# Kernel tuning notes

Measured on AMD Instinct MI355X. Metric: run time of the kernel, lower is better.

Reference implementation:

```python
import jax, jax.numpy as jnp
import numpy as np

N_NODES = 100000
N_EDGES = 1600000
HIDDEN = 64
N_LAYERS = 3
N_CLASSES = 2
N_GRAPHS = 128
NEG_SLOPE = 0.2  # PyG GATConv default negative_slope


def setup_inputs() -> dict:
    key = jax.random.key(0)
    ks = jax.random.split(key, 8)
    x = jax.random.randint(ks[0], (N_NODES,), 0, 2)
    edge_index = jax.random.randint(ks[1], (2, N_EDGES), 0, N_NODES)
    batch = jnp.sort(jax.random.randint(ks[2], (N_NODES,), 0, N_GRAPHS))
    scale = 1.0 / np.sqrt(HIDDEN)
    embed_table = jax.random.normal(ks[3], (2, HIDDEN), jnp.float32)
    Ws = jax.random.normal(ks[4], (N_LAYERS, HIDDEN, HIDDEN), jnp.float32) * scale
    a_srcs = jax.random.normal(ks[5], (N_LAYERS, HIDDEN), jnp.float32) * scale
    a_dsts = jax.random.normal(ks[6], (N_LAYERS, HIDDEN), jnp.float32) * scale
    biases = jnp.zeros((N_LAYERS, HIDDEN), jnp.float32)
    W_out = jax.random.normal(ks[7], (HIDDEN, N_CLASSES), jnp.float32) * scale
    b_out = jnp.zeros((N_CLASSES,), jnp.float32)
    return {"x": x, "edge_index": edge_index, "batch": batch,
            "embed_table": embed_table, "Ws": Ws, "a_srcs": a_srcs,
            "a_dsts": a_dsts, "biases": biases, "W_out": W_out, "b_out": b_out}


def _gat_layer(h, src, dst, W, a_s, a_d, b):
    # h: [N, D]; src/dst: [E'] (self loops included) -> PyG GATConv, heads=1
    hW = h @ W                                   # [N, D]
    e = jax.nn.leaky_relu((hW @ a_s)[src] + (hW @ a_d)[dst], NEG_SLOPE)  # [E']
    m = jax.ops.segment_max(e, dst, num_segments=N_NODES)               # stable softmax per dst
    ex = jnp.exp(e - m[dst])
    denom = jax.ops.segment_sum(ex, dst, num_segments=N_NODES)
    alpha = ex / denom[dst]                      # [E']
    out = jax.ops.segment_sum(hW[src] * alpha[:, None], dst, num_segments=N_NODES)
    return out + b


def reference(x, edge_index, batch, embed_table, Ws, a_srcs, a_dsts, biases, W_out, b_out):
    loop = jnp.arange(N_NODES)
    src = jnp.concatenate([edge_index[0], loop])  # PyG add_self_loops=True
    dst = jnp.concatenate([edge_index[1], loop])
    h = embed_table[x]                            # [N, D]
    for l in range(N_LAYERS):
        h = _gat_layer(h, src, dst, Ws[l], a_srcs[l], a_dsts[l], biases[l])
        if l < N_LAYERS - 1:
            h = jax.nn.relu(h)
    sums = jax.ops.segment_sum(h, batch, num_segments=N_GRAPHS)
    counts = jax.ops.segment_sum(jnp.ones((N_NODES,), h.dtype), batch, num_segments=N_GRAPHS)
    pooled = sums / jnp.maximum(counts, 1.0)[:, None]  # global_mean_pool
    return pooled @ W_out + b_out                      # [G, num_classes]
```

## Files before the change

kernel.cpp:

```cpp
#include <hip/hip_runtime.h>
#include <hip/hip_bf16.h>
#include <float.h>

#define N_NODES 100000
#define N_EDGES 1600000
#define HIDDEN 64
#define N_GRAPHS 128
#define NEG_SLOPE 0.2f
#define ETOT (N_EDGES + N_NODES)

#define BSHIFT 9
#define NB ((N_NODES + 511) >> BSHIFT)
#define PAIR_CHUNK 4096
#define PAIR_BLOCKS ((N_EDGES + PAIR_CHUNK - 1) / PAIR_CHUNK)
#define XBIT_BLOCKS ((N_NODES + 255) / 256)
#define TBL_BLOCKS (NLVL / 4)
#define CAP 12288

#define NREP 64
#define REP_STRIDE 272
#define NLVL 512

__device__ __forceinline__ unsigned short f2bf(float f) {
    unsigned u = __float_as_uint(f);
    unsigned r = (u + 0x7FFFu + ((u >> 16) & 1u)) >> 16;
    return (unsigned short)r;
}
__device__ __forceinline__ float blo(unsigned u) { return __uint_as_float(u << 16); }
__device__ __forceinline__ float bhi(unsigned u) { return __uint_as_float(u & 0xFFFF0000u); }
__device__ __forceinline__ int sb0(unsigned u) { return (int)((unsigned)(u << 24)) >> 24; }
__device__ __forceinline__ int sb1(unsigned u) { return (int)((unsigned)(u << 16)) >> 24; }
__device__ __forceinline__ int sb2(unsigned u) { return (int)((unsigned)(u << 8)) >> 24; }
__device__ __forceinline__ int sb3(unsigned u) { return (int)u >> 24; }


__global__ __launch_bounds__(256) void k_prep(
    const int* __restrict__ x,
    const float* __restrict__ embed, const float* __restrict__ Ws,
    const float* __restrict__ biases, const float* __restrict__ a_srcs,
    const float* __restrict__ a_dsts, const float* __restrict__ W_out,
    int* __restrict__ gcnt, float* __restrict__ pool_acc,
    unsigned* __restrict__ xb,
    unsigned char* __restrict__ Tq8, float* __restrict__ Tscl,
    float* __restrict__ Ts1s, float* __restrict__ Ts1d,
    float* __restrict__ sparams)
{
    int t = threadIdx.x, b = blockIdx.x;

    if (b < TBL_BLOCKS) {
        if (b == 0 && t < NB) gcnt[t] = 0;
        if (b < NREP && t < 2 * N_GRAPHS) pool_acc[b * REP_STRIDE + t] = 0.f;

        int l = b * 4 + (t >> 6);
        int f = t & 63;
        float r0 = 0.f, r1 = 0.f;
#pragma unroll 8
        for (int k = 0; k < 64; ++k) {
            float w = Ws[k * 64 + f];
            r0 = fmaf(embed[k], w, r0);
            r1 = fmaf(embed[64 + k], w, r1);
        }
        if (l == 0) {
            float as = a_srcs[f], ad = a_dsts[f];
            float t0 = r0 * as, t1 = r1 * as, t2 = r0 * ad, t3 = r1 * ad;
#pragma unroll
            for (int off = 32; off >= 1; off >>= 1) {
                t0 += __shfl_xor(t0, off); t1 += __shfl_xor(t1, off);
                t2 += __shfl_xor(t2, off); t3 += __shfl_xor(t3, off);
            }
            if (f == 0) { sparams[0] = t0; sparams[1] = t1; sparams[2] = t2; sparams[3] = t3; }
        }
        if (l == 1) {
            float b2 = biases[128 + f];
            float t4 = b2 * W_out[f * 2];
            float t5 = b2 * W_out[f * 2 + 1];
#pragma unroll
            for (int off = 32; off >= 1; off >>= 1) {
                t4 += __shfl_xor(t4, off); t5 += __shfl_xor(t5, off);
            }
            if (f == 0) { sparams[4] = t4; sparams[5] = t5; }
        }
        float c1 = (float)l * (1.f / (NLVL - 1));
        float o = fmaxf(biases[f] + r0 + c1 * (r1 - r0), 0.f);
        const float* W1 = Ws + 4096;
        float h = 0.f;
#pragma unroll 8
        for (int k = 0; k < 64; ++k) h = fmaf(__shfl(o, k), W1[k * 64 + f], h);
        float ss = h * a_srcs[64 + f];
        float sd = h * a_dsts[64 + f];
        float am = fabsf(h);
#pragma unroll
        for (int off = 32; off >= 1; off >>= 1) {
            ss += __shfl_xor(ss, off);
            sd += __shfl_xor(sd, off);
            am = fmaxf(am, __shfl_xor(am, off));
        }
        float iscl = (am > 0.f) ? 127.f / am : 0.f;
        Tq8[l * 64 + f] = (unsigned char)(__float2int_rn(h * iscl) & 255);
        if (f == 0) { Tscl[l] = am * (1.f / 127.f); Ts1s[l] = ss; Ts1d[l] = sd; }
    } else {
        int i = (b - TBL_BLOCKS) * 256 + t;
        int lane = t & 63;
        bool bb = (i < N_NODES) && (x[i] != 0);
        unsigned long long m = __ballot(bb);
        int wid = i >> 6;
        if (i < N_NODES + 64) {
            if (lane == 0) xb[wid * 2] = (unsigned)m;
            if (lane == 32) xb[wid * 2 + 1] = (unsigned)(m >> 32);
        }
    }
}


__global__ __launch_bounds__(256) void k_scatter(
    const int* __restrict__ e0, const int* __restrict__ e1,
    const unsigned* __restrict__ xb, int* __restrict__ gcnt,
    int* __restrict__ pairs)
{
    __shared__ int hcnt[NB];
    __shared__ int base[NB];
    __shared__ int lstart[NB];
    __shared__ int tot[256];
    __shared__ int staged[PAIR_CHUNK];
    __shared__ int sdest[PAIR_CHUNK];
    int t = threadIdx.x, b = blockIdx.x;
    if (t < NB) hcnt[t] = 0;
    __syncthreads();
    int ebase = b * PAIR_CHUNK;
    int ecount = min(PAIR_CHUNK, N_EDGES - ebase);
    for (int i = 4 * t; i < ecount; i += 1024) {
        int4 d4 = *(const int4*)(e1 + ebase + i);
        atomicAdd(&hcnt[d4.x >> BSHIFT], 1);
        atomicAdd(&hcnt[d4.y >> BSHIFT], 1);
        atomicAdd(&hcnt[d4.z >> BSHIFT], 1);
        atomicAdd(&hcnt[d4.w >> BSHIFT], 1);
    }
    __syncthreads();
    int v = (t < NB) ? hcnt[t] : 0;
    tot[t] = v;
    __syncthreads();
    for (int off = 1; off < 256; off <<= 1) {
        int u = (t >= off) ? tot[t - off] : 0;
        __syncthreads();
        tot[t] += u;
        __syncthreads();
    }
    if (t < NB) {
        lstart[t] = tot[t] - v;
        base[t] = v ? atomicAdd(&gcnt[t], v) : 0;
        hcnt[t] = 0;
    }
    __syncthreads();
    for (int i = 4 * t; i < ecount; i += 1024) {
        int4 s4 = *(const int4*)(e0 + ebase + i);
        int4 d4 = *(const int4*)(e1 + ebase + i);
        int ss[4] = {s4.x, s4.y, s4.z, s4.w};
        int dd[4] = {d4.x, d4.y, d4.z, d4.w};
#pragma unroll
        for (int j = 0; j < 4; ++j) {
            int s = ss[j], d = dd[j];
            int xv = (xb[s >> 5] >> (s & 31)) & 1;
            int B = d >> BSHIFT;
            int idx = atomicAdd(&hcnt[B], 1);
            int lp = lstart[B] + idx;
            staged[lp] = (xv << 26) | ((d & 511) << 17) | s;
            sdest[lp] = B * CAP + base[B] + idx;
        }
    }
    __syncthreads();
    for (int i = t; i < ecount; i += 256)
        pairs[sdest[i]] = staged[i];
}

__global__ __launch_bounds__(1024) void k_csr_bucket(
    const int* __restrict__ pairs, const int* __restrict__ gcnt,
    const int* __restrict__ x, const float* __restrict__ sparams,
    int* __restrict__ rowptr, int* __restrict__ col,
    unsigned short* __restrict__ cidx)
{
    __shared__ int deg[512];
    __shared__ int excl[512];
    __shared__ int cnt2[512];
    __shared__ int wsum[16];
    __shared__ int p0sh;
    int b = blockIdx.x;
    int t = threadIdx.x;
    int nb = b << BSHIFT;
    int nodes = min(512, N_NODES - nb);

    int pv = (t < b) ? gcnt[t] : 0;
#pragma unroll
    for (int off = 32; off >= 1; off >>= 1) pv += __shfl_xor(pv, off);
    if ((t & 63) == 0) wsum[t >> 6] = pv;
    __syncthreads();
    if (t == 0) {
        int s = 0;
#pragma unroll
        for (int i = 0; i < 16; ++i) s += wsum[i];
        p0sh = s;
    }

    int xself = 0;
    if (t < 512) {
        xself = (t < nodes) ? (x[nb + t] & 1) : 0;
        deg[t] = (t < nodes) ? (1 | (xself << 16)) : 0;
        cnt2[t] = 1;
    }
    __syncthreads();
    int cnt = gcnt[b];
    int pbase = b * CAP;
    for (int i = t; i < cnt; i += 1024) {
        int p = pairs[pbase + i];
        atomicAdd(&deg[(p >> 17) & 511], 1 | (((p >> 26) & 1) << 16));
    }
    __syncthreads();

    int packed = (t < 512) ? deg[t] : 0;
    int val = packed & 0xFFFF;
    int kx = packed >> 16;
    if (t < nodes) {
        float ss0 = sparams[0], ss1 = sparams[1];
        float sd = xself ? sparams[3] : sparams[2];
        float e0 = ss0 + sd; e0 = (e0 >= 0.f) ? e0 : NEG_SLOPE * e0;
        float e1 = ss1 + sd; e1 = (e1 >= 0.f) ? e1 : NEG_SLOPE * e1;
        float pp0 = __expf(e0), pp1 = __expf(e1);
        float kn = (float)kx, dn = (float)(val - kx);
        float c1 = kn * pp1 / (dn * pp0 + kn * pp1);
        cidx[nb + t] = (unsigned short)__float2int_rn(c1 * (float)(NLVL - 1));
    }

    int xx = val;
#pragma unroll
    for (int off = 1; off < 64; off <<= 1) {
        int y = __shfl_up(xx, off);
        if ((t & 63) >= off) xx += y;
    }
    if ((t & 63) == 63 && t < 512) wsum[t >> 6] = xx;
    __syncthreads();
    if (t == 0) {
        int s = 0;
#pragma unroll
        for (int i = 0; i < 8; ++i) { int v = wsum[i]; wsum[i] = s; s += v; }
    }
    __syncthreads();
    int ex = xx - val + wsum[t >> 6];
    if (t < 512) excl[t] = ex;

    int p0 = p0sh;
    int colbase = p0 + nb;
    if (t < nodes) {
        rowptr[nb + t] = colbase + ex;
        col[colbase + ex] = nb + t;
    }
    if (b == NB - 1 && t == 0) rowptr[N_NODES] = ETOT;
    __syncthreads();
    for (int i = t; i < cnt; i += 1024) {
        int p = pairs[pbase + i];
        int li = (p >> 17) & 511;
        int pos = colbase + excl[li] + atomicAdd(&cnt2[li], 1);
        col[pos] = p & 0x1FFFF;
    }
}


__global__ __launch_bounds__(256) void k_agg1(
    const unsigned char* __restrict__ Tq8, const float* __restrict__ Tscl,
    const float* __restrict__ Ts1s, const float* __restrict__ Ts1d,
    const unsigned short* __restrict__ cidx, const int* __restrict__ col,
    const int* __restrict__ rowptr, const float* __restrict__ bias,
    unsigned short* __restrict__ hout)
{
    __shared__ float2 stash[4][64];
    int t = threadIdx.x;
    int wave = t >> 6, lane = t & 63;
    int h = lane >> 5, hl = lane & 31;
    int base = blockIdx.x * 8 + wave * 2;
    if (base >= N_NODES) return;
    const char* hb = (const char*)Tq8;

    int node = base + h;
    bool valid = (node < N_NODES);
    int row = 0, end = 0;
    if (valid) { row = rowptr[node]; end = rowptr[node + 1]; }
    int deg = end - row;
    int degO = __shfl_xor(deg, 32);
    bool fast = (deg <= 32) && (degO <= 32);

    if (fast) {
        int idx = 0;
        float p = 0.f, sc = 0.f;
        if (hl < deg) idx = cidx[col[row + hl]];
        float sdi = Ts1d[__shfl(idx, h * 32)];
        if (hl < deg) {
            float ee = Ts1s[idx] + sdi;
            ee = (ee >= 0.f) ? ee : NEG_SLOPE * ee;
            p = __expf(ee);
            sc = Tscl[idx];
        }
        stash[wave][lane] = make_float2(p * sc, __int_as_float(idx * 64));

        int q = hl >> 4;
        int f = hl & 15;
        int f4 = f * 4;
        int sb = h * 32;
        float a0 = 0.f, a1 = 0.f, a2 = 0.f, a3 = 0.f;
        int degr = (deg + 7) & ~7;
        for (int j = q; j < degr; j += 8) {
            float2 e0 = stash[wave][sb + j];
            float2 e1 = stash[wave][sb + j + 2];
            float2 e2 = stash[wave][sb + j + 4];
            float2 e3 = stash[wave][sb + j + 6];
            unsigned v0 = *(const unsigned*)(hb + (__float_as_int(e0.y) + f4));
            unsigned v1 = *(const unsigned*)(hb + (__float_as_int(e1.y) + f4));
            unsigned v2 = *(const unsigned*)(hb + (__float_as_int(e2.y) + f4));
            unsigned v3 = *(const unsigned*)(hb + (__float_as_int(e3.y) + f4));
            a0 = fmaf(e0.x, (float)sb0(v0), a0);
            a1 = fmaf(e0.x, (float)sb1(v0), a1);
            a2 = fmaf(e0.x, (float)sb2(v0), a2);
            a3 = fmaf(e0.x, (float)sb3(v0), a3);
            a0 = fmaf(e1.x, (float)sb0(v1), a0);
            a1 = fmaf(e1.x, (float)sb1(v1), a1);
            a2 = fmaf(e1.x, (float)sb2(v1), a2);
            a3 = fmaf(e1.x, (float)sb3(v1), a3);
            a0 = fmaf(e2.x, (float)sb0(v2), a0);
            a1 = fmaf(e2.x, (float)sb1(v2), a1);
            a2 = fmaf(e2.x, (float)sb2(v2), a2);
            a3 = fmaf(e2.x, (float)sb3(v2), a3);
            a0 = fmaf(e3.x, (float)sb0(v3), a0);
            a1 = fmaf(e3.x, (float)sb1(v3), a1);
            a2 = fmaf(e3.x, (float)sb2(v3), a2);
            a3 = fmaf(e3.x, (float)sb3(v3), a3);
        }
        float denom = p;
#pragma unroll
        for (int off = 16; off >= 1; off >>= 1) denom += __shfl_xor(denom, off);
        float inv = 1.f / denom;
        a0 += __shfl_xor(a0, 16);
        a1 += __shfl_xor(a1, 16);
        a2 += __shfl_xor(a2, 16);
        a3 += __shfl_xor(a3, 16);
        if (hl < 16 && valid) {
            float4 bb = *(const float4*)&bias[4 * f];
            ushort4 pk;
            pk.x = f2bf(fmaxf(fmaf(a0, inv, bb.x), 0.f));
            pk.y = f2bf(fmaxf(fmaf(a1, inv, bb.y), 0.f));
            pk.z = f2bf(fmaxf(fmaf(a2, inv, bb.z), 0.f));
            pk.w = f2bf(fmaxf(fmaf(a3, inv, bb.w), 0.f));
            *(ushort4*)&hout[node * 64 + 4 * f] = pk;
        }
    } else {
        for (int s = 0; s < 2; ++s) {
            int nd = base + s;
            if (nd >= N_NODES) continue;
            int r = rowptr[nd], e = rowptr[nd + 1];
            float sdi = Ts1d[cidx[nd]];
            float m = -FLT_MAX;
            for (int j = r + lane; j < e; j += 64) {
                float ee = Ts1s[cidx[col[j]]] + sdi;
                ee = (ee >= 0.f) ? ee : NEG_SLOPE * ee;
                m = fmaxf(m, ee);
            }
#pragma unroll
            for (int off = 32; off >= 1; off >>= 1) m = fmaxf(m, __shfl_xor(m, off));
            float denom = 0.f;
            for (int j = r + lane; j < e; j += 64) {
                float ee = Ts1s[cidx[col[j]]] + sdi;
                ee = (ee >= 0.f) ? ee : NEG_SLOPE * ee;
                denom += __expf(ee - m);
            }
#pragma unroll
            for (int off = 32; off >= 1; off >>= 1) denom += __shfl_xor(denom, off);
            float inv = 1.f / denom;
            float acc = 0.f;
            for (int j = r; j < e; ++j) {
                int idxj = cidx[col[j]];
                float ee = Ts1s[idxj] + sdi;
                ee = (ee >= 0.f) ? ee : NEG_SLOPE * ee;
                float w = __expf(ee - m) * inv * Tscl[idxj];
                int bq = (int)(signed char)Tq8[idxj * 64 + lane];
                acc = fmaf(w, (float)bq, acc);
            }
            hout[nd * 64 + lane] = f2bf(fmaxf(acc + bias[lane], 0.f));
        }
    }
}


__global__ __launch_bounds__(256) void k_gemm2(
    const unsigned* __restrict__ h32, const float* __restrict__ W,
    const float* __restrict__ a_s, const float* __restrict__ a_d,
    const float* __restrict__ W_out,
    float4* __restrict__ szz)
{
    __shared__ float Wl[64 * 64];
    __shared__ float hT[64 * 68];
    int t = threadIdx.x;
    int r0 = blockIdx.x * 64;

    for (int i = t; i < 4096; i += 256) Wl[i] = W[i];
    for (int i = t; i < 2048; i += 256) {
        int r = i >> 5, m = i & 31;
        int row = r0 + r;
        unsigned u = (row < N_NODES) ? h32[row * 32 + m] : 0u;
        hT[(2 * m) * 68 + r]     = blo(u);
        hT[(2 * m + 1) * 68 + r] = bhi(u);
    }
    __syncthreads();

    int tcol = t & 15;
    int trow = t >> 4;
    float acc[4][4];
#pragma unroll
    for (int i = 0; i < 4; ++i)
#pragma unroll
        for (int j = 0; j < 4; ++j) acc[i][j] = 0.f;

    for (int k = 0; k < 64; ++k) {
        float4 va = *(const float4*)&hT[k * 68 + trow * 4];
        float4 vb = *(const float4*)&Wl[k * 64 + tcol * 4];
        float a[4] = {va.x, va.y, va.z, va.w};
        float bb[4] = {vb.x, vb.y, vb.z, vb.w};
#pragma unroll
        for (int i = 0; i < 4; ++i)
#pragma unroll
            for (int j = 0; j < 4; ++j) acc[i][j] = fmaf(a[i], bb[j], acc[i][j]);
    }

    float4 as4 = *(const float4*)&a_s[tcol * 4];
    float4 ad4 = *(const float4*)&a_d[tcol * 4];
    float asr[4] = {as4.x, as4.y, as4.z, as4.w};
    float adr[4] = {ad4.x, ad4.y, ad4.z, ad4.w};
    float4 wa = *(const float4*)&W_out[8 * tcol];
    float4 wb = *(const float4*)&W_out[8 * tcol + 4];

#pragma unroll
    for (int i = 0; i < 4; ++i) {
        int row = r0 + trow * 4 + i;
        float ps = 0.f, pd = 0.f;
#pragma unroll
        for (int j = 0; j < 4; ++j) {
            ps = fmaf(acc[i][j], asr[j], ps);
            pd = fmaf(acc[i][j], adr[j], pd);
        }
        float z0 = acc[i][0] * wa.x + acc[i][1] * wa.z + acc[i][2] * wb.x + acc[i][3] * wb.z;
        float z1 = acc[i][0] * wa.y + acc[i][1] * wa.w + acc[i][2] * wb.y + acc[i][3] * wb.w;
#pragma unroll
        for (int off = 8; off >= 1; off >>= 1) {
            ps += __shfl_xor(ps, off);
            pd += __shfl_xor(pd, off);
            z0 += __shfl_xor(z0, off);
            z1 += __shfl_xor(z1, off);
        }
        if (row < N_NODES && tcol == 0) {
            szz[row] = make_float4(ps, z0, z1, pd);
        }
    }
}


__global__ __launch_bounds__(256) void k_pool2(
    const float4* __restrict__ szz, const int* __restrict__ col,
    const int* __restrict__ rowptr, const int* __restrict__ batch,
    float* __restrict__ pool_acc)
{
    __shared__ int rp2[33];
    int t = threadIdx.x;
    int wave = t >> 6, lane = t & 63;
    int h = lane >> 5, hl = lane & 31;
    int nb0 = blockIdx.x * 32;
    if (t < 33) {
        int n = nb0 + t;
        rp2[t] = (n <= N_NODES) ? rowptr[n] : ETOT;
    }
    __syncthreads();
    float* rep = pool_acc + ((blockIdx.x * 4 + wave) & (NREP - 1)) * REP_STRIDE;

    int gcur = -1;
    float acc0 = 0.f, acc1 = 0.f;

#pragma unroll
    for (int i = 0; i < 4; ++i) {
        int nls = wave * 8 + 2 * i + h;
        int node = nb0 + nls;
        bool valid = (node < N_NODES);
        int row = valid ? rp2[nls] : 0;
        int end = valid ? rp2[nls + 1] : 0;
        int deg = end - row;
        int degO = __shfl_xor(deg, 32);
        bool fast = (deg <= 32) && (degO <= 32);
        float r0 = 0.f, r1 = 0.f;

        if (fast) {
            float sdi = valid ? szz[node].w : 0.f;
            float p = 0.f, zy = 0.f, zz = 0.f;
            if (hl < deg) {
                int c = col[row + hl];
                float4 sz = szz[c];
                float ee = sz.x + sdi;
                ee = (ee >= 0.f) ? ee : NEG_SLOPE * ee;
                p = __expf(ee);
                zy = sz.y; zz = sz.z;
            }
            float n0 = p * zy, n1 = p * zz, dn = p;
#pragma unroll
            for (int off = 16; off >= 1; off >>= 1) {
                n0 += __shfl_xor(n0, off);
                n1 += __shfl_xor(n1, off);
                dn += __shfl_xor(dn, off);
            }
            float inv = 1.f / dn;
            r0 = n0 * inv; r1 = n1 * inv;
        } else {
            float rr0[2], rr1[2];
#pragma unroll
            for (int s = 0; s < 2; ++s) {
                rr0[s] = rr1[s] = 0.f;
                int nds = wave * 8 + 2 * i + s;
                int nd = nb0 + nds;
                if (nd >= N_NODES) continue;
                int r = rp2[nds], e = rp2[nds + 1];
                float sdi = szz[nd].w;
                float n0 = 0.f, n1 = 0.f, dn = 0.f;
                for (int j = r + lane; j < e; j += 64) {
                    int c = col[j];
                    float4 sz = szz[c];
                    float ee = sz.x + sdi;
                    ee = (ee >= 0.f) ? ee : NEG_SLOPE * ee;
                    float p = __expf(ee);
                    n0 = fmaf(p, sz.y, n0);
                    n1 = fmaf(p, sz.z, n1);
                    dn += p;
                }
#pragma unroll
                for (int off = 32; off >= 1; off >>= 1) {
                    n0 += __shfl_xor(n0, off);
                    n1 += __shfl_xor(n1, off);
                    dn += __shfl_xor(dn, off);
                }
                float inv = 1.f / dn;
                rr0[s] = n0 * inv; rr1[s] = n1 * inv;
            }
            r0 = rr0[h]; r1 = rr1[h];
        }

        if (hl == 0 && valid) {
            int g = batch[node];
            if (g != gcur) {
                if (gcur >= 0) {
                    atomicAdd(&rep[gcur * 2], acc0);
                    atomicAdd(&rep[gcur * 2 + 1], acc1);
                }
                gcur = g; acc0 = r0; acc1 = r1;
            } else {
                acc0 += r0; acc1 += r1;
            }
        }
    }
    if (hl == 0 && gcur >= 0) {
        atomicAdd(&rep[gcur * 2], acc0);
        atomicAdd(&rep[gcur * 2 + 1], acc1);
    }
}


__device__ __forceinline__ int lower_bound_dev(const int* __restrict__ a, int n, int v) {
    int lo = 0, hi = n;
    while (lo < hi) {
        int mid = (lo + hi) >> 1;
        if (a[mid] < v) lo = mid + 1; else hi = mid;
    }
    return lo;
}

__global__ void k_head(const float* __restrict__ pool_acc,
                       const int* __restrict__ batch,
                       const float* __restrict__ b_out,
                       const float* __restrict__ sparams,
                       float* __restrict__ out)
{
    int t = threadIdx.x;
    if (t < 2 * N_GRAPHS) {
        float s = 0.f;
#pragma unroll 8
        for (int r = 0; r < NREP; ++r) s += pool_acc[r * REP_STRIDE + t];
        int g = t >> 1, c = t & 1;
        int start = lower_bound_dev(batch, N_NODES, g);
        int end = lower_bound_dev(batch, N_NODES, g + 1);
        float cnt = fmaxf((float)(end - start), 1.f);
        out[t] = s / cnt + sparams[4 + c] + b_out[c];
    }
}


extern "C" void kernel_launch(void* const* d_in, const int* in_sizes, int n_in,
                              void* d_out, int out_size, void* d_ws, size_t ws_size,
                              hipStream_t stream) {
    const int*   x       = (const int*)d_in[0];
    const int*   edge    = (const int*)d_in[1];
    const int*   batch   = (const int*)d_in[2];
    const float* embed   = (const float*)d_in[3];
    const float* Ws      = (const float*)d_in[4];
    const float* a_srcs  = (const float*)d_in[5];
    const float* a_dsts  = (const float*)d_in[6];
    const float* biases  = (const float*)d_in[7];
    const float* W_out   = (const float*)d_in[8];
    const float* b_out   = (const float*)d_in[9];
    float* out = (float*)d_out;

    char* ws = (char*)d_ws;
    size_t off = 0;
    auto alloc = [&](size_t bytes) -> void* {
        void* p = ws + off;
        off += (bytes + 255) & ~(size_t)255;
        return p;
    };
    unsigned short* hout  = (unsigned short*)alloc((size_t)N_NODES * 64 * sizeof(unsigned short));
    float4* szz     = (float4*)alloc((size_t)N_NODES * sizeof(float4));
    unsigned short* cidx = (unsigned short*)alloc((size_t)N_NODES * sizeof(unsigned short));
    int*   rowptr   = (int*)alloc((size_t)(N_NODES + 1) * sizeof(int));
    int*   colA     = (int*)alloc((size_t)ETOT * sizeof(int));
    int*   gcnt     = (int*)alloc((size_t)NB * sizeof(int));
    float* pool_acc = (float*)alloc((size_t)(NREP * REP_STRIDE) * sizeof(float));
    unsigned* xb    = (unsigned*)alloc((size_t)3232 * sizeof(unsigned));
    unsigned char* Tq8 = (unsigned char*)alloc((size_t)NLVL * 64);
    float* Tscl     = (float*)alloc((size_t)NLVL * sizeof(float));
    float* Ts1s     = (float*)alloc((size_t)NLVL * sizeof(float));
    float* Ts1d     = (float*)alloc((size_t)NLVL * sizeof(float));
    float* sparams  = (float*)alloc((size_t)8 * sizeof(float));
    int*   pairs    = (int*)alloc((size_t)NB * CAP * sizeof(int));

    const int* e0 = edge;
    const int* e1 = edge + N_EDGES;

    k_prep<<<TBL_BLOCKS + XBIT_BLOCKS, 256, 0, stream>>>(
        x, embed, Ws, biases, a_srcs, a_dsts, W_out,
        gcnt, pool_acc, xb, Tq8, Tscl, Ts1s, Ts1d, sparams);
    k_scatter<<<PAIR_BLOCKS, 256, 0, stream>>>(e0, e1, xb, gcnt, pairs);
    k_csr_bucket<<<NB, 1024, 0, stream>>>(pairs, gcnt, x, sparams, rowptr, colA, cidx);

    k_agg1<<<(N_NODES + 7) / 8, 256, 0, stream>>>(
        Tq8, Tscl, Ts1s, Ts1d, cidx, colA, rowptr, biases + 64, hout);
    k_gemm2<<<(N_NODES + 63) / 64, 256, 0, stream>>>(
        (const unsigned*)hout, Ws + 8192, a_srcs + 128, a_dsts + 128, W_out, szz);
    k_pool2<<<(N_NODES + 31) / 32, 256, 0, stream>>>(
        szz, colA, rowptr, batch, pool_acc);
    k_head<<<1, 256, 0, stream>>>(pool_acc, batch, b_out, sparams, out);
}
```

Before: 203.3 us.

## Move table precompute into scatter kernel, widen scatter blocks, vectorize bucket reads

The layer-1 lookup table computation moves out of k_prep into extra blocks of k_scatter, leaving k_prep to do only zeroing and bit-packing. k_scatter now runs 512-thread blocks over each 4096-edge chunk. k_csr_bucket reads the pairs array as int4 in both passes. The aim is to take the table work off the critical path ahead of scatter, and to cut per-thread loop iterations and load instructions, at the cost of higher per-block shared-memory atomic contention.

```diff
diff --git a/kernel.cpp b/kernel.cpp
--- a/kernel.cpp
+++ b/kernel.cpp
@@ -14,7 +14,7 @@
 #define PAIR_CHUNK 4096
 #define PAIR_BLOCKS ((N_EDGES + PAIR_CHUNK - 1) / PAIR_CHUNK)
 #define XBIT_BLOCKS ((N_NODES + 255) / 256)
-#define TBL_BLOCKS (NLVL / 4)
+#define TBL_BLOCKS (NLVL / 8)
 #define CAP 12288
 
 #define NREP 64
@@ -36,22 +36,45 @@
 
 __global__ __launch_bounds__(256) void k_prep(
     const int* __restrict__ x,
+    int* __restrict__ gcnt, float* __restrict__ pool_acc,
+    unsigned* __restrict__ xb)
+{
+    int t = threadIdx.x, b = blockIdx.x;
+    if (b == 0 && t < NB) gcnt[t] = 0;
+    if (b < NREP && t < 2 * N_GRAPHS) pool_acc[b * REP_STRIDE + t] = 0.f;
+    int i = b * 256 + t;
+    int lane = t & 63;
+    bool bb = (i < N_NODES) && (x[i] != 0);
+    unsigned long long m = __ballot(bb);
+    int wid = i >> 6;
+    if (i < N_NODES + 64) {
+        if (lane == 0) xb[wid * 2] = (unsigned)m;
+        if (lane == 32) xb[wid * 2 + 1] = (unsigned)(m >> 32);
+    }
+}
+
+
+__global__ __launch_bounds__(512) void k_scatter(
+    const int* __restrict__ e0, const int* __restrict__ e1,
+    const unsigned* __restrict__ xb, int* __restrict__ gcnt,
+    int* __restrict__ pairs,
     const float* __restrict__ embed, const float* __restrict__ Ws,
     const float* __restrict__ biases, const float* __restrict__ a_srcs,
     const float* __restrict__ a_dsts, const float* __restrict__ W_out,
-    int* __restrict__ gcnt, float* __restrict__ pool_acc,
-    unsigned* __restrict__ xb,
     unsigned char* __restrict__ Tq8, float* __restrict__ Tscl,
     float* __restrict__ Ts1s, float* __restrict__ Ts1d,
     float* __restrict__ sparams)
 {
+    __shared__ int hcnt[NB];
+    __shared__ int base[NB];
+    __shared__ int lstart[NB];
+    __shared__ int tot[256];
+    __shared__ int staged[PAIR_CHUNK];
+    __shared__ int sdest[PAIR_CHUNK];
     int t = threadIdx.x, b = blockIdx.x;
 
-    if (b < TBL_BLOCKS) {
-        if (b == 0 && t < NB) gcnt[t] = 0;
-        if (b < NREP && t < 2 * N_GRAPHS) pool_acc[b * REP_STRIDE + t] = 0.f;
-
-        int l = b * 4 + (t >> 6);
+    if (b >= PAIR_BLOCKS) {
+        int l = (b - PAIR_BLOCKS) * 8 + (t >> 6);
         int f = t & 63;
         float r0 = 0.f, r1 = 0.f;
 #pragma unroll 8
@@ -98,37 +121,14 @@
         float iscl = (am > 0.f) ? 127.f / am : 0.f;
         Tq8[l * 64 + f] = (unsigned char)(__float2int_rn(h * iscl) & 255);
         if (f == 0) { Tscl[l] = am * (1.f / 127.f); Ts1s[l] = ss; Ts1d[l] = sd; }
-    } else {
-        int i = (b - TBL_BLOCKS) * 256 + t;
-        int lane = t & 63;
-        bool bb = (i < N_NODES) && (x[i] != 0);
-        unsigned long long m = __ballot(bb);
-        int wid = i >> 6;
-        if (i < N_NODES + 64) {
-            if (lane == 0) xb[wid * 2] = (unsigned)m;
-            if (lane == 32) xb[wid * 2 + 1] = (unsigned)(m >> 32);
-        }
-    }
-}
-
-
-__global__ __launch_bounds__(256) void k_scatter(
-    const int* __restrict__ e0, const int* __restrict__ e1,
-    const unsigned* __restrict__ xb, int* __restrict__ gcnt,
-    int* __restrict__ pairs)
-{
-    __shared__ int hcnt[NB];
-    __shared__ int base[NB];
-    __shared__ int lstart[NB];
-    __shared__ int tot[256];
-    __shared__ int staged[PAIR_CHUNK];
-    __shared__ int sdest[PAIR_CHUNK];
-    int t = threadIdx.x, b = blockIdx.x;
+        return;
+    }
+
     if (t < NB) hcnt[t] = 0;
     __syncthreads();
     int ebase = b * PAIR_CHUNK;
     int ecount = min(PAIR_CHUNK, N_EDGES - ebase);
-    for (int i = 4 * t; i < ecount; i += 1024) {
+    for (int i = 4 * t; i < ecount; i += 2048) {
         int4 d4 = *(const int4*)(e1 + ebase + i);
         atomicAdd(&hcnt[d4.x >> BSHIFT], 1);
         atomicAdd(&hcnt[d4.y >> BSHIFT], 1);
@@ -137,12 +137,12 @@
     }
     __syncthreads();
     int v = (t < NB) ? hcnt[t] : 0;
-    tot[t] = v;
+    if (t < 256) tot[t] = v;
     __syncthreads();
     for (int off = 1; off < 256; off <<= 1) {
-        int u = (t >= off) ? tot[t - off] : 0;
+        int u = (t >= off && t < 256) ? tot[t - off] : 0;
         __syncthreads();
-        tot[t] += u;
+        if (t < 256) tot[t] += u;
         __syncthreads();
     }
     if (t < NB) {
@@ -151,7 +151,7 @@
         hcnt[t] = 0;
     }
     __syncthreads();
-    for (int i = 4 * t; i < ecount; i += 1024) {
+    for (int i = 4 * t; i < ecount; i += 2048) {
         int4 s4 = *(const int4*)(e0 + ebase + i);
         int4 d4 = *(const int4*)(e1 + ebase + i);
         int ss[4] = {s4.x, s4.y, s4.z, s4.w};
@@ -168,7 +168,7 @@
         }
     }
     __syncthreads();
-    for (int i = t; i < ecount; i += 256)
+    for (int i = t; i < ecount; i += 512)
         pairs[sdest[i]] = staged[i];
 }
 
@@ -209,7 +209,15 @@
     __syncthreads();
     int cnt = gcnt[b];
     int pbase = b * CAP;
-    for (int i = t; i < cnt; i += 1024) {
+    int cnt4 = cnt & ~3;
+    for (int i = 4 * t; i < cnt4; i += 4096) {
+        int4 p4 = *(const int4*)(pairs + pbase + i);
+        atomicAdd(&deg[(p4.x >> 17) & 511], 1 | (((p4.x >> 26) & 1) << 16));
+        atomicAdd(&deg[(p4.y >> 17) & 511], 1 | (((p4.y >> 26) & 1) << 16));
+        atomicAdd(&deg[(p4.z >> 17) & 511], 1 | (((p4.z >> 26) & 1) << 16));
+        atomicAdd(&deg[(p4.w >> 17) & 511], 1 | (((p4.w >> 26) & 1) << 16));
+    }
+    for (int i = cnt4 + t; i < cnt; i += 1024) {
         int p = pairs[pbase + i];
         atomicAdd(&deg[(p >> 17) & 511], 1 | (((p >> 26) & 1) << 16));
     }
@@ -254,7 +262,17 @@
     }
     if (b == NB - 1 && t == 0) rowptr[N_NODES] = ETOT;
     __syncthreads();
-    for (int i = t; i < cnt; i += 1024) {
+    for (int i = 4 * t; i < cnt4; i += 4096) {
+        int4 p4 = *(const int4*)(pairs + pbase + i);
+        int pp[4] = {p4.x, p4.y, p4.z, p4.w};
+#pragma unroll
+        for (int j = 0; j < 4; ++j) {
+            int li = (pp[j] >> 17) & 511;
+            int pos = colbase + excl[li] + atomicAdd(&cnt2[li], 1);
+            col[pos] = pp[j] & 0x1FFFF;
+        }
+    }
+    for (int i = cnt4 + t; i < cnt; i += 1024) {
         int p = pairs[pbase + i];
         int li = (p >> 17) & 511;
         int pos = colbase + excl[li] + atomicAdd(&cnt2[li], 1);
@@ -632,10 +650,11 @@
     const int* e0 = edge;
     const int* e1 = edge + N_EDGES;
 
-    k_prep<<<TBL_BLOCKS + XBIT_BLOCKS, 256, 0, stream>>>(
-        x, embed, Ws, biases, a_srcs, a_dsts, W_out,
-        gcnt, pool_acc, xb, Tq8, Tscl, Ts1s, Ts1d, sparams);
-    k_scatter<<<PAIR_BLOCKS, 256, 0, stream>>>(e0, e1, xb, gcnt, pairs);
+    k_prep<<<XBIT_BLOCKS, 256, 0, stream>>>(x, gcnt, pool_acc, xb);
+    k_scatter<<<PAIR_BLOCKS + TBL_BLOCKS, 512, 0, stream>>>(
+        e0, e1, xb, gcnt, pairs,
+        embed, Ws, biases, a_srcs, a_dsts, W_out,
+        Tq8, Tscl, Ts1s, Ts1d, sparams);
     k_csr_bucket<<<NB, 1024, 0, stream>>>(pairs, gcnt, x, sparams, rowptr, colA, cidx);
 
     k_agg1<<<(N_NODES + 7) / 8, 256, 0, stream>>>(
```

Measured after the change: 198.4 us. 1.02x faster.
